# Kernel tuning notes

Hardware: AMD Instinct MI355X
Metric: run time of the kernel (lower is better)

## Reference

```python
import jax, jax.numpy as jnp
import numpy as np

B, N, C = 4, 49152, 256
E = 393216
CMID = C // 4
K = 3
EPS = 1e-5


def _cheb_prop(x, row, col, a_norm):
    # L_hat x with lambda_max=2, sym norm: L_hat = -D^{-1/2} A D^{-1/2} (zero diag)
    # x: [B, N, F]
    msg = a_norm[None, :, None] * x[:, col, :]           # [B, E, F]
    return -jnp.zeros_like(x).at[:, row, :].add(msg)


def _cheb_conv(x, row, col, a_norm, W, b):
    # W: [K, Fin, Fout], b: [Fout]
    out = jnp.einsum('bnf,fg->bng', x, W[0])
    Tx0, Tx1 = x, _cheb_prop(x, row, col, a_norm)
    out = out + jnp.einsum('bnf,fg->bng', Tx1, W[1])
    for k in range(2, W.shape[0]):
        Tx2 = 2.0 * _cheb_prop(Tx1, row, col, a_norm) - Tx0
        out = out + jnp.einsum('bnf,fg->bng', Tx2, W[k])
        Tx0, Tx1 = Tx1, Tx2
    return out + b


def _inst_norm(y):
    # InstanceNorm over the node axis (y viewed as [B, C, N]), affine=False
    mean = jnp.mean(y, axis=1, keepdims=True)
    var = jnp.var(y, axis=1, keepdims=True)
    return (y - mean) * jax.lax.rsqrt(var + EPS)


def setup_inputs() -> dict:
    key = jax.random.key(0)
    ks = jax.random.split(key, 8)
    x = jax.random.normal(ks[0], (B, N, C), dtype=jnp.float32)
    edge_index = jax.random.randint(ks[1], (2, E), 0, N, dtype=jnp.int32)
    edge_weight = jax.random.uniform(ks[2], (E,), dtype=jnp.float32)
    s1 = 1.0 / np.sqrt(C)
    s2 = 1.0 / np.sqrt(CMID)
    W1 = jax.random.normal(ks[3], (K, C, CMID), dtype=jnp.float32) * s1
    W2 = jax.random.normal(ks[4], (K, CMID, CMID), dtype=jnp.float32) * s2
    W3 = jax.random.normal(ks[5], (K, CMID, C), dtype=jnp.float32) * s2
    b1 = jnp.zeros((CMID,), dtype=jnp.float32)
    b2 = jnp.zeros((CMID,), dtype=jnp.float32)
    b3 = jnp.zeros((C,), dtype=jnp.float32)
    return {"x": x, "edge_index": edge_index, "edge_weight": edge_weight,
            "W1": W1, "b1": b1, "W2": W2, "b2": b2, "W3": W3, "b3": b3}


def reference(x, edge_index, edge_weight, W1, b1, W2, b2, W3, b3):
    row, col = edge_index[0], edge_index[1]
    deg = jnp.zeros((N,), dtype=x.dtype).at[row].add(edge_weight)
    dinv = jnp.where(deg > 0, jax.lax.rsqrt(jnp.maximum(deg, EPS)), 0.0)
    a_norm = edge_weight * dinv[row] * dinv[col]

    y = _cheb_conv(x, row, col, a_norm, W1, b1)
    y = jax.nn.relu(_inst_norm(y))
    y = _cheb_conv(y, row, col, a_norm, W2, b2)
    y = jax.nn.relu(_inst_norm(y))
    y = _cheb_conv(y, row, col, a_norm, W3, b3)
    y = jax.nn.relu(_inst_norm(y))
    return y + x
```

## Files before the change

### kernel.cpp

```cpp
#include <hip/hip_runtime.h>

#define NNODES 49152
#define NB 4
#define NE 393216
#define MTOT (NB*NNODES)
#define EPS 1e-5f

typedef __attribute__((ext_vector_type(8))) short s8v;
typedef __attribute__((ext_vector_type(4))) float f32x4;

__device__ inline float b2f(ushort u){ union{uint i; float f;} v; v.i = ((uint)u)<<16; return v.f; }
__device__ inline ushort f2b(float f){ union{float f; uint i;} v; v.f=f; uint r = v.i + 0x7fff + ((v.i>>16)&1); return (ushort)(r>>16); }

__global__ __launch_bounds__(256) void k_deg_cnt(const int* __restrict__ row,
    const float* __restrict__ w, float* __restrict__ deg, int* __restrict__ cnt)
{
    int e = blockIdx.x*256 + threadIdx.x;
    if (e >= NE) return;
    int r = row[e];
    atomicAdd(&deg[r], w[e]);
    atomicAdd(&cnt[r], 1);
}

__global__ __launch_bounds__(256) void k_dinv(const float* __restrict__ deg, float* __restrict__ dinv)
{
    int i = blockIdx.x*256 + threadIdx.x;
    if (i >= NNODES) return;
    float d = deg[i];
    dinv[i] = (d > 0.0f) ? rsqrtf(fmaxf(d, EPS)) : 0.0f;
}

__global__ __launch_bounds__(1024) void k_scan(const int* __restrict__ cnt, int* __restrict__ rowptr)
{
    __shared__ int ssum[1024];
    const int CH = NNODES/1024;
    int t = threadIdx.x;
    int base = t*CH;
    int loc[CH];
    int s = 0;
    #pragma unroll
    for (int i = 0; i < CH; ++i) { loc[i] = s; s += cnt[base+i]; }
    ssum[t] = s;
    __syncthreads();
    for (int off = 1; off < 1024; off <<= 1) {
        int v = ssum[t];
        int add = (t >= off) ? ssum[t-off] : 0;
        __syncthreads();
        ssum[t] = v + add;
        __syncthreads();
    }
    int prefix = (t == 0) ? 0 : ssum[t-1];
    #pragma unroll
    for (int i = 0; i < CH; ++i) rowptr[base+i] = prefix + loc[i];
    if (t == 0) rowptr[NNODES] = ssum[1023];
}

__global__ __launch_bounds__(256) void k_fill(const int* __restrict__ row, const int* __restrict__ col,
    const float* __restrict__ w, const float* __restrict__ dinv,
    const int* __restrict__ rowptr, int* __restrict__ fill,
    int* __restrict__ ecol, float* __restrict__ ea)
{
    int e = blockIdx.x*256 + threadIdx.x;
    if (e >= NE) return;
    int r = row[e], c = col[e];
    int pos = rowptr[r] + atomicAdd(&fill[r], 1);
    ecol[pos] = c;
    ea[pos] = w[e] * dinv[r] * dinv[c];
}

__global__ __launch_bounds__(256) void k_packB(const float* __restrict__ W, int Fin, int NF, int K,
    int mode, ushort* __restrict__ out)
{
    int t = blockIdx.x*256 + threadIdx.x;
    int lane = t & 63;
    int fid = t >> 6;
    if (fid >= (K/32)*NF) return;
    int kb = fid / NF, nb = fid % NF;
    int kbase = kb*32 + ((lane>>4)<<3);
    int n0 = nb*16 + (lane&15);
    #pragma unroll
    for (int j = 0; j < 8; ++j) {
        int kk = kbase + j;
        float v;
        if (mode == 0) {
            if (n0 < 64)       v = W[kk*64 + n0] - W[2*Fin*64 + kk*64 + n0];
            else if (n0 < 128) v = W[Fin*64 + kk*64 + (n0-64)];
            else               v = W[2*Fin*64 + kk*64 + (n0-128)];
        } else {
            v = W[(kk>>6)*64*256 + (kk&63)*256 + n0];
        }
        out[((long)fid*64 + lane)*8 + j] = f2b(v);
    }
}

template<int N_, int AF32, int OUTF32>
__global__ __launch_bounds__(256) void k_mgemm(
    const void* __restrict__ A0v, const void* __restrict__ A1v, const void* __restrict__ A2v,
    int Kper, int K, const ushort* __restrict__ Bp, void* __restrict__ Cv)
{
    const int NF = N_/16;
    int tid = threadIdx.x;
    int w = tid >> 6, l = tid & 63;
    long row_base = (long)blockIdx.x*128 + w*32;
    int lr = l & 15;
    int kg = l >> 4;
    f32x4 acc[2][NF];
    #pragma unroll
    for (int rf = 0; rf < 2; ++rf)
        #pragma unroll
        for (int nb = 0; nb < NF; ++nb) acc[rf][nb] = (f32x4){0.f,0.f,0.f,0.f};

    for (int kt = 0; kt < K; kt += 32) {
        int part = kt / Kper;
        const void* Ap = (part == 0) ? A0v : ((part == 1) ? A1v : A2v);
        int kc = kt - part*Kper;
        s8v afr[2];
        #pragma unroll
        for (int rf = 0; rf < 2; ++rf) {
            long row = row_base + rf*16 + lr;
            if (AF32) {
                const float* af = (const float*)Ap + row*(long)Kper + kc + (kg<<3);
                float4 v0 = *(const float4*)af;
                float4 v1 = *(const float4*)(af + 4);
                s8v fr;
                fr[0]=(short)f2b(v0.x); fr[1]=(short)f2b(v0.y); fr[2]=(short)f2b(v0.z); fr[3]=(short)f2b(v0.w);
                fr[4]=(short)f2b(v1.x); fr[5]=(short)f2b(v1.y); fr[6]=(short)f2b(v1.z); fr[7]=(short)f2b(v1.w);
                afr[rf] = fr;
            } else {
                afr[rf] = *(const s8v*)((const ushort*)Ap + row*(long)Kper + kc + (kg<<3));
            }
        }
        const ushort* bb = Bp + ((long)(kt>>5)*NF*64 + l)*8;
        #pragma unroll
        for (int nb = 0; nb < NF; ++nb) {
            s8v bfr = *(const s8v*)(bb + (long)nb*64*8);
            acc[0][nb] = __builtin_amdgcn_mfma_f32_16x16x32_bf16(afr[0], bfr, acc[0][nb], 0, 0, 0);
            acc[1][nb] = __builtin_amdgcn_mfma_f32_16x16x32_bf16(afr[1], bfr, acc[1][nb], 0, 0, 0);
        }
    }
    #pragma unroll
    for (int rf = 0; rf < 2; ++rf) {
        long r0 = row_base + rf*16 + (kg<<2);
        #pragma unroll
        for (int nb = 0; nb < NF; ++nb) {
            int cc = nb*16 + lr;
            #pragma unroll
            for (int i = 0; i < 4; ++i) {
                float v = acc[rf][nb][i];
                if (OUTF32) ((float*)Cv)[(r0+i)*N_ + cc] = v;
                else        ((ushort*)Cv)[(r0+i)*N_ + cc] = f2b(v);
            }
        }
    }
}

__global__ __launch_bounds__(256) void k_prop(
    const int* __restrict__ rowptr, const int* __restrict__ ecol, const float* __restrict__ ea,
    const ushort* __restrict__ src, int sstride, int soff,
    const ushort* __restrict__ basep, int bstride, int boff, float beta,
    ushort* __restrict__ dst, int dstride, int doff, float alpha)
{
    int g = blockIdx.x*16 + (threadIdx.x >> 4);
    int q = threadIdx.x & 15;
    int e0 = rowptr[g], e1 = rowptr[g+1];
    f32x4 acc[4];
    #pragma unroll
    for (int b = 0; b < 4; ++b) acc[b] = (f32x4){0.f,0.f,0.f,0.f};
    for (int e = e0; e < e1; ++e) {
        int c = ecol[e];
        float a = ea[e];
        #pragma unroll
        for (int b = 0; b < 4; ++b) {
            ushort4 v = *(const ushort4*)(src + ((long)b*NNODES + c)*sstride + soff + q*4);
            acc[b][0] += a*b2f(v.x); acc[b][1] += a*b2f(v.y);
            acc[b][2] += a*b2f(v.z); acc[b][3] += a*b2f(v.w);
        }
    }
    #pragma unroll
    for (int b = 0; b < 4; ++b) {
        float r0 = alpha*acc[b][0], r1 = alpha*acc[b][1], r2 = alpha*acc[b][2], r3 = alpha*acc[b][3];
        if (basep) {
            ushort4 bb = *(const ushort4*)(basep + ((long)b*NNODES + g)*bstride + boff + q*4);
            r0 += beta*b2f(bb.x); r1 += beta*b2f(bb.y); r2 += beta*b2f(bb.z); r3 += beta*b2f(bb.w);
        }
        ushort4 o; o.x = f2b(r0); o.y = f2b(r1); o.z = f2b(r2); o.w = f2b(r3);
        *(ushort4*)(dst + ((long)b*NNODES + g)*dstride + doff + q*4) = o;
    }
}

__global__ __launch_bounds__(256) void k_stats64(const ushort* __restrict__ y,
    float* __restrict__ sum, float* __restrict__ sumsq)
{
    int b = blockIdx.y;
    int c4 = (threadIdx.x & 15)*4;
    int rsub = threadIdx.x >> 4;
    long r0 = (long)blockIdx.x*256;
    float s0=0,s1=0,s2=0,s3=0, q0=0,q1=0,q2=0,q3=0;
    for (int i = 0; i < 16; ++i) {
        long r = r0 + rsub + i*16;
        ushort4 v = *(const ushort4*)(y + ((long)b*NNODES + r)*192 + c4);
        float f0=b2f(v.x), f1=b2f(v.y), f2=b2f(v.z), f3=b2f(v.w);
        s0+=f0; q0+=f0*f0; s1+=f1; q1+=f1*f1; s2+=f2; q2+=f2*f2; s3+=f3; q3+=f3*f3;
    }
    __shared__ float ls[16][64], lss[16][64];
    ls[rsub][c4]=s0; ls[rsub][c4+1]=s1; ls[rsub][c4+2]=s2; ls[rsub][c4+3]=s3;
    lss[rsub][c4]=q0; lss[rsub][c4+1]=q1; lss[rsub][c4+2]=q2; lss[rsub][c4+3]=q3;
    __syncthreads();
    for (int off = 8; off; off >>= 1) {
        if (rsub < off) {
            #pragma unroll
            for (int j = 0; j < 4; ++j) {
                ls[rsub][c4+j] += ls[rsub+off][c4+j];
                lss[rsub][c4+j] += lss[rsub+off][c4+j];
            }
        }
        __syncthreads();
    }
    if (rsub == 0) {
        #pragma unroll
        for (int j = 0; j < 4; ++j) {
            atomicAdd(&sum[b*256 + c4 + j], ls[0][c4+j]);
            atomicAdd(&sumsq[b*256 + c4 + j], lss[0][c4+j]);
        }
    }
}

__global__ __launch_bounds__(256) void k_stats256(const float* __restrict__ y,
    float* __restrict__ sum, float* __restrict__ sumsq)
{
    int b = blockIdx.y;
    int c = threadIdx.x;
    long r0 = (long)blockIdx.x*256;
    float s = 0.f, ss = 0.f;
    for (int r = 0; r < 256; ++r) {
        float v = y[((long)b*NNODES + r0 + r)*256 + c];
        s += v; ss += v*v;
    }
    atomicAdd(&sum[b*256 + c], s);
    atomicAdd(&sumsq[b*256 + c], ss);
}

__global__ __launch_bounds__(256) void k_finalize(const float* __restrict__ sum,
    const float* __restrict__ sumsq, float* __restrict__ mean, float* __restrict__ rs, int C_)
{
    int i = blockIdx.x*256 + threadIdx.x;
    if (i >= NB*256) return;
    int c = i % 256;
    if (c >= C_) return;
    float m = sum[i] / (float)NNODES;
    float v = sumsq[i] / (float)NNODES - m*m;
    mean[i] = m;
    rs[i] = rsqrtf(v + EPS);
}

__global__ __launch_bounds__(256) void k_normrelu(const ushort* __restrict__ U,
    const float* __restrict__ mean, const float* __restrict__ rs, ushort* __restrict__ X)
{
    long idx = (long)blockIdx.x*256 + threadIdx.x;
    long bn = idx >> 4;
    int q = (int)(idx & 15);
    int b = (int)(bn / NNODES);
    ushort4 v = *(const ushort4*)(U + bn*192 + q*4);
    float4 m = *(const float4*)(mean + b*256 + q*4);
    float4 r_ = *(const float4*)(rs + b*256 + q*4);
    ushort4 o;
    o.x = f2b(fmaxf((b2f(v.x)-m.x)*r_.x, 0.f));
    o.y = f2b(fmaxf((b2f(v.y)-m.y)*r_.y, 0.f));
    o.z = f2b(fmaxf((b2f(v.z)-m.z)*r_.z, 0.f));
    o.w = f2b(fmaxf((b2f(v.w)-m.w)*r_.w, 0.f));
    *(ushort4*)(X + bn*64 + q*4) = o;
}

__global__ __launch_bounds__(256) void k_final(float* __restrict__ Y,
    const float* __restrict__ x, const float* __restrict__ mean, const float* __restrict__ rs)
{
    long idx = (long)blockIdx.x*256 + threadIdx.x;
    long bn = idx >> 6;
    int q = (int)(idx & 63);
    int b = (int)(bn / NNODES);
    float4 v = *(const float4*)(Y + bn*256 + q*4);
    float4 m = *(const float4*)(mean + b*256 + q*4);
    float4 r_ = *(const float4*)(rs + b*256 + q*4);
    float4 xv = *(const float4*)(x + bn*256 + q*4);
    float4 o;
    o.x = fmaxf((v.x-m.x)*r_.x, 0.f) + xv.x;
    o.y = fmaxf((v.y-m.y)*r_.y, 0.f) + xv.y;
    o.z = fmaxf((v.z-m.z)*r_.z, 0.f) + xv.z;
    o.w = fmaxf((v.w-m.w)*r_.w, 0.f) + xv.w;
    *(float4*)(Y + bn*256 + q*4) = o;
}

extern "C" void kernel_launch(void* const* d_in, const int* in_sizes, int n_in,
                              void* d_out, int out_size, void* d_ws, size_t ws_size,
                              hipStream_t stream)
{
    const float* x  = (const float*)d_in[0];
    const int*   ei = (const int*)d_in[1];
    const float* ew = (const float*)d_in[2];
    const float* W1 = (const float*)d_in[3];
    const float* W2 = (const float*)d_in[5];
    const float* W3 = (const float*)d_in[7];
    const int* row = ei;
    const int* col = ei + NE;

    char* p = (char*)d_ws;
    size_t used = 0;
    auto alloc = [&](size_t bytes) -> void* {
        void* r = p + used;
        used += (bytes + 1023) & ~(size_t)1023;
        return r;
    };
    float* deg   = (float*)alloc((size_t)3*NNODES*4);
    int*   cnt   = (int*)(deg + NNODES);
    int*   fillc = (int*)(deg + 2*NNODES);
    float* dinv  = (float*)alloc((size_t)NNODES*4);
    int*   rowptr= (int*)alloc((size_t)(NNODES+1)*4);
    int*   ecol  = (int*)alloc((size_t)NE*4);
    float* ea    = (float*)alloc((size_t)NE*4);
    float* stats = (float*)alloc((size_t)2*NB*256*4);
    float* sumb  = stats;
    float* sumsq = stats + NB*256;
    float* meanb = (float*)alloc((size_t)NB*256*4);
    float* rsb   = (float*)alloc((size_t)NB*256*4);
    ushort* Bp1  = (ushort*)alloc((size_t)256*192*2);
    ushort* Bp2  = (ushort*)alloc((size_t)64*192*2);
    ushort* Bp3  = (ushort*)alloc((size_t)192*256*2);
    ushort* bufX = (ushort*)alloc((size_t)MTOT*64*2);
    ushort* T1   = (ushort*)alloc((size_t)MTOT*64*2);
    ushort* T2   = (ushort*)alloc((size_t)MTOT*64*2);
    if (ws_size < used) return;

    ushort* U = (ushort*)d_out;
    float*  Y = (float*)d_out;

    hipMemsetAsync(deg, 0, (size_t)3*NNODES*4, stream);
    k_deg_cnt<<<NE/256, 256, 0, stream>>>(row, ew, deg, cnt);
    k_dinv<<<NNODES/256, 256, 0, stream>>>(deg, dinv);
    k_scan<<<1, 1024, 0, stream>>>(cnt, rowptr);
    k_fill<<<NE/256, 256, 0, stream>>>(row, col, ew, dinv, rowptr, fillc, ecol, ea);
    k_packB<<<24, 256, 0, stream>>>(W1, 256, 12, 256, 0, Bp1);
    k_packB<<<6, 256, 0, stream>>>(W2, 64, 12, 64, 0, Bp2);
    k_packB<<<24, 256, 0, stream>>>(W3, 64, 16, 192, 1, Bp3);

    k_mgemm<192,1,0><<<MTOT/128, 256, 0, stream>>>(x, nullptr, nullptr, 256, 256, Bp1, U);
    k_prop<<<NNODES/16, 256, 0, stream>>>(rowptr, ecol, ea, U,192,128, U,192,64, 1.f, U,192,64, -2.f);
    k_prop<<<NNODES/16, 256, 0, stream>>>(rowptr, ecol, ea, U,192,64,  U,192,0,  1.f, U,192,0,  -1.f);
    hipMemsetAsync(stats, 0, (size_t)2*NB*256*4, stream);
    k_stats64<<<dim3(NNODES/256, NB), 256, 0, stream>>>(U, sumb, sumsq);
    k_finalize<<<NB, 256, 0, stream>>>(sumb, sumsq, meanb, rsb, 64);
    k_normrelu<<<MTOT*16/256, 256, 0, stream>>>(U, meanb, rsb, bufX);

    k_mgemm<192,0,0><<<MTOT/128, 256, 0, stream>>>(bufX, nullptr, nullptr, 64, 64, Bp2, U);
    k_prop<<<NNODES/16, 256, 0, stream>>>(rowptr, ecol, ea, U,192,128, U,192,64, 1.f, U,192,64, -2.f);
    k_prop<<<NNODES/16, 256, 0, stream>>>(rowptr, ecol, ea, U,192,64,  U,192,0,  1.f, U,192,0,  -1.f);
    hipMemsetAsync(stats, 0, (size_t)2*NB*256*4, stream);
    k_stats64<<<dim3(NNODES/256, NB), 256, 0, stream>>>(U, sumb, sumsq);
    k_finalize<<<NB, 256, 0, stream>>>(sumb, sumsq, meanb, rsb, 64);
    k_normrelu<<<MTOT*16/256, 256, 0, stream>>>(U, meanb, rsb, bufX);

    k_prop<<<NNODES/16, 256, 0, stream>>>(rowptr, ecol, ea, bufX,64,0, (const ushort*)nullptr,0,0, 0.f, T1,64,0, -1.f);
    k_prop<<<NNODES/16, 256, 0, stream>>>(rowptr, ecol, ea, T1,64,0, bufX,64,0, -1.f, T2,64,0, -2.f);
    k_mgemm<256,0,1><<<MTOT/128, 256, 0, stream>>>(bufX, T1, T2, 64, 192, Bp3, Y);
    hipMemsetAsync(stats, 0, (size_t)2*NB*256*4, stream);
    k_stats256<<<dim3(NNODES/256, NB), 256, 0, stream>>>(Y, sumb, sumsq);
    k_finalize<<<NB, 256, 0, stream>>>(sumb, sumsq, meanb, rsb, 256);
    k_final<<<MTOT*64/256, 256, 0, stream>>>(Y, x, meanb, rsb);
}
```

Before: 698.9 us.

## Interleave batch into node rows and split GEMM outputs into separate buffers

Intermediate activations move to a node-major layout with the 4 batches interleaved, [N][B][64]. One propagation row therefore gathers a contiguous 512-byte segment per edge instead of four strided segments, and the Chebyshev terms are written by the GEMM into separate contiguous buffers. Stats and normalization kernels are rewritten for the new layout with wider vector loads, and the stat memsets are merged into the initial one. When workspace allows, the final GEMM output is kept as bf16 in a workspace buffer and the last norm kernel reads it back, transposing to the batch-major output. This adds index remapping and a second code path in exchange.

```diff
diff --git a/kernel.cpp b/kernel.cpp
--- a/kernel.cpp
+++ b/kernel.cpp
@@ -93,17 +93,17 @@
     }
 }
 
-template<int N_, int AF32, int OUTF32>
+template<int N_, int AMODE, int CMODE>
 __global__ __launch_bounds__(256) void k_mgemm(
-    const void* __restrict__ A0v, const void* __restrict__ A1v, const void* __restrict__ A2v,
-    int Kper, int K, const ushort* __restrict__ Bp, void* __restrict__ Cv)
+    const void* __restrict__ Aa, const void* __restrict__ Ab, const void* __restrict__ Ac,
+    int K, const ushort* __restrict__ Bp,
+    void* __restrict__ C0, void* __restrict__ C1, void* __restrict__ C2)
 {
     const int NF = N_/16;
     int tid = threadIdx.x;
     int w = tid >> 6, l = tid & 63;
-    long row_base = (long)blockIdx.x*128 + w*32;
-    int lr = l & 15;
-    int kg = l >> 4;
+    int lr = l & 15, kg = l >> 4;
+    long rb = (long)blockIdx.x * 128;
     f32x4 acc[2][NF];
     #pragma unroll
     for (int rf = 0; rf < 2; ++rf)
@@ -111,44 +111,57 @@
         for (int nb = 0; nb < NF; ++nb) acc[rf][nb] = (f32x4){0.f,0.f,0.f,0.f};
 
     for (int kt = 0; kt < K; kt += 32) {
-        int part = kt / Kper;
-        const void* Ap = (part == 0) ? A0v : ((part == 1) ? A1v : A2v);
-        int kc = kt - part*Kper;
         s8v afr[2];
         #pragma unroll
         for (int rf = 0; rf < 2; ++rf) {
-            long row = row_base + rf*16 + lr;
-            if (AF32) {
-                const float* af = (const float*)Ap + row*(long)Kper + kc + (kg<<3);
+            long rg = rb + w*32 + rf*16 + lr;
+            if (AMODE == 1) {
+                const float* af = (const float*)Aa + rg*256 + kt + (kg<<3);
                 float4 v0 = *(const float4*)af;
                 float4 v1 = *(const float4*)(af + 4);
                 s8v fr;
                 fr[0]=(short)f2b(v0.x); fr[1]=(short)f2b(v0.y); fr[2]=(short)f2b(v0.z); fr[3]=(short)f2b(v0.w);
                 fr[4]=(short)f2b(v1.x); fr[5]=(short)f2b(v1.y); fr[6]=(short)f2b(v1.z); fr[7]=(short)f2b(v1.w);
                 afr[rf] = fr;
+            } else if (AMODE == 0) {
+                afr[rf] = *(const s8v*)((const ushort*)Aa + rg*64 + kt + (kg<<3));
             } else {
-                afr[rf] = *(const s8v*)((const ushort*)Ap + row*(long)Kper + kc + (kg<<3));
+                int part = kt >> 6, kc = kt & 63;
+                const ushort* ap = (part == 0) ? (const ushort*)Aa : ((part == 1) ? (const ushort*)Ab : (const ushort*)Ac);
+                afr[rf] = *(const s8v*)(ap + rg*64 + kc + (kg<<3));
             }
         }
-        const ushort* bb = Bp + ((long)(kt>>5)*NF*64 + l)*8;
+        const ushort* bb = Bp + ((long)(kt>>5)*NF)*512 + l*8;
         #pragma unroll
         for (int nb = 0; nb < NF; ++nb) {
-            s8v bfr = *(const s8v*)(bb + (long)nb*64*8);
+            s8v bfr = *(const s8v*)(bb + nb*512);
             acc[0][nb] = __builtin_amdgcn_mfma_f32_16x16x32_bf16(afr[0], bfr, acc[0][nb], 0, 0, 0);
             acc[1][nb] = __builtin_amdgcn_mfma_f32_16x16x32_bf16(afr[1], bfr, acc[1][nb], 0, 0, 0);
         }
     }
+
+    int b4 = 0, n0 = 0;
+    if (AMODE == 1) { b4 = (int)(rb / NNODES); n0 = (int)(rb - (long)b4*NNODES); }
     #pragma unroll
     for (int rf = 0; rf < 2; ++rf) {
-        long r0 = row_base + rf*16 + (kg<<2);
         #pragma unroll
         for (int nb = 0; nb < NF; ++nb) {
-            int cc = nb*16 + lr;
             #pragma unroll
             for (int i = 0; i < 4; ++i) {
+                int lrw = w*32 + rf*16 + kg*4 + i;
+                int cc = nb*16 + lr;
                 float v = acc[rf][nb][i];
-                if (OUTF32) ((float*)Cv)[(r0+i)*N_ + cc] = v;
-                else        ((ushort*)Cv)[(r0+i)*N_ + cc] = f2b(v);
+                if (CMODE == 0) {
+                    long crow = (AMODE == 1) ? ((long)(n0 + lrw)*4 + b4) : (rb + lrw);
+                    ushort* arr = (nb < 4) ? (ushort*)C0 : ((nb < 8) ? (ushort*)C1 : (ushort*)C2);
+                    arr[crow*64 + (nb&3)*16 + lr] = f2b(v);
+                } else if (CMODE == 1) {
+                    ((ushort*)C0)[(rb + lrw)*256 + cc] = f2b(v);
+                } else {
+                    long r = rb + lrw;
+                    int n = (int)(r >> 2), b = (int)(r & 3);
+                    ((float*)C0)[((long)b*NNODES + n)*256 + cc] = v;
+                }
             }
         }
     }
@@ -156,88 +169,99 @@
 
 __global__ __launch_bounds__(256) void k_prop(
     const int* __restrict__ rowptr, const int* __restrict__ ecol, const float* __restrict__ ea,
-    const ushort* __restrict__ src, int sstride, int soff,
-    const ushort* __restrict__ basep, int bstride, int boff, float beta,
-    ushort* __restrict__ dst, int dstride, int doff, float alpha)
-{
-    int g = blockIdx.x*16 + (threadIdx.x >> 4);
-    int q = threadIdx.x & 15;
+    const ushort* __restrict__ src, const ushort* __restrict__ basep, float beta,
+    ushort* __restrict__ dst, float alpha)
+{
+    int g = blockIdx.x*8 + (threadIdx.x >> 5);
+    int sub = threadIdx.x & 31;
     int e0 = rowptr[g], e1 = rowptr[g+1];
-    f32x4 acc[4];
-    #pragma unroll
-    for (int b = 0; b < 4; ++b) acc[b] = (f32x4){0.f,0.f,0.f,0.f};
+    float acc[8];
+    #pragma unroll
+    for (int j = 0; j < 8; ++j) acc[j] = 0.f;
     for (int e = e0; e < e1; ++e) {
         int c = ecol[e];
         float a = ea[e];
-        #pragma unroll
-        for (int b = 0; b < 4; ++b) {
-            ushort4 v = *(const ushort4*)(src + ((long)b*NNODES + c)*sstride + soff + q*4);
-            acc[b][0] += a*b2f(v.x); acc[b][1] += a*b2f(v.y);
-            acc[b][2] += a*b2f(v.z); acc[b][3] += a*b2f(v.w);
-        }
-    }
-    #pragma unroll
-    for (int b = 0; b < 4; ++b) {
-        float r0 = alpha*acc[b][0], r1 = alpha*acc[b][1], r2 = alpha*acc[b][2], r3 = alpha*acc[b][3];
-        if (basep) {
-            ushort4 bb = *(const ushort4*)(basep + ((long)b*NNODES + g)*bstride + boff + q*4);
-            r0 += beta*b2f(bb.x); r1 += beta*b2f(bb.y); r2 += beta*b2f(bb.z); r3 += beta*b2f(bb.w);
-        }
-        ushort4 o; o.x = f2b(r0); o.y = f2b(r1); o.z = f2b(r2); o.w = f2b(r3);
-        *(ushort4*)(dst + ((long)b*NNODES + g)*dstride + doff + q*4) = o;
-    }
-}
-
-__global__ __launch_bounds__(256) void k_stats64(const ushort* __restrict__ y,
+        s8v v = *(const s8v*)(src + (long)c*256 + sub*8);
+        #pragma unroll
+        for (int j = 0; j < 8; ++j) acc[j] += a * b2f((ushort)v[j]);
+    }
+    s8v o;
+    if (basep) {
+        s8v bv = *(const s8v*)(basep + (long)g*256 + sub*8);
+        #pragma unroll
+        for (int j = 0; j < 8; ++j) o[j] = (short)f2b(alpha*acc[j] + beta*b2f((ushort)bv[j]));
+    } else {
+        #pragma unroll
+        for (int j = 0; j < 8; ++j) o[j] = (short)f2b(alpha*acc[j]);
+    }
+    *(s8v*)(dst + (long)g*256 + sub*8) = o;
+}
+
+__global__ __launch_bounds__(256) void k_statsA(const ushort* __restrict__ y,
     float* __restrict__ sum, float* __restrict__ sumsq)
 {
-    int b = blockIdx.y;
-    int c4 = (threadIdx.x & 15)*4;
-    int rsub = threadIdx.x >> 4;
-    long r0 = (long)blockIdx.x*256;
-    float s0=0,s1=0,s2=0,s3=0, q0=0,q1=0,q2=0,q3=0;
-    for (int i = 0; i < 16; ++i) {
-        long r = r0 + rsub + i*16;
-        ushort4 v = *(const ushort4*)(y + ((long)b*NNODES + r)*192 + c4);
-        float f0=b2f(v.x), f1=b2f(v.y), f2=b2f(v.z), f3=b2f(v.w);
-        s0+=f0; q0+=f0*f0; s1+=f1; q1+=f1*f1; s2+=f2; q2+=f2*f2; s3+=f3; q3+=f3*f3;
-    }
-    __shared__ float ls[16][64], lss[16][64];
-    ls[rsub][c4]=s0; ls[rsub][c4+1]=s1; ls[rsub][c4+2]=s2; ls[rsub][c4+3]=s3;
-    lss[rsub][c4]=q0; lss[rsub][c4+1]=q1; lss[rsub][c4+2]=q2; lss[rsub][c4+3]=q3;
+    int t = threadIdx.x;
+    float s[8], q[8];
+    #pragma unroll
+    for (int j = 0; j < 8; ++j) { s[j] = 0.f; q[j] = 0.f; }
+    for (int i = 0; i < 12; ++i) {
+        long e = ((long)(i*512 + blockIdx.x))*2048 + t*8;
+        s8v v = *(const s8v*)(y + e);
+        #pragma unroll
+        for (int j = 0; j < 8; ++j) { float f = b2f((ushort)v[j]); s[j] += f; q[j] += f*f; }
+    }
+    __shared__ float ls[256][8], lq[256][8];
+    #pragma unroll
+    for (int j = 0; j < 8; ++j) { ls[t][j] = s[j]; lq[t][j] = q[j]; }
     __syncthreads();
-    for (int off = 8; off; off >>= 1) {
-        if (rsub < off) {
+    #pragma unroll
+    for (int off = 128; off >= 32; off >>= 1) {
+        if (t < off) {
             #pragma unroll
-            for (int j = 0; j < 4; ++j) {
-                ls[rsub][c4+j] += ls[rsub+off][c4+j];
-                lss[rsub][c4+j] += lss[rsub+off][c4+j];
-            }
+            for (int j = 0; j < 8; ++j) { ls[t][j] += ls[t+off][j]; lq[t][j] += lq[t+off][j]; }
         }
         __syncthreads();
     }
-    if (rsub == 0) {
-        #pragma unroll
-        for (int j = 0; j < 4; ++j) {
-            atomicAdd(&sum[b*256 + c4 + j], ls[0][c4+j]);
-            atomicAdd(&sumsq[b*256 + c4 + j], lss[0][c4+j]);
-        }
-    }
-}
-
-__global__ __launch_bounds__(256) void k_stats256(const float* __restrict__ y,
+    if (t < 32) {
+        int b = (t>>3)&3, c0 = (t&7)*8;
+        #pragma unroll
+        for (int j = 0; j < 8; ++j) {
+            atomicAdd(&sum[b*256 + c0 + j], ls[t][j]);
+            atomicAdd(&sumsq[b*256 + c0 + j], lq[t][j]);
+        }
+    }
+}
+
+__global__ __launch_bounds__(256) void k_statsY(const ushort* __restrict__ y,
     float* __restrict__ sum, float* __restrict__ sumsq)
 {
-    int b = blockIdx.y;
-    int c = threadIdx.x;
-    long r0 = (long)blockIdx.x*256;
-    float s = 0.f, ss = 0.f;
-    for (int r = 0; r < 256; ++r) {
-        float v = y[((long)b*NNODES + r0 + r)*256 + c];
-        s += v; ss += v*v;
-    }
-    atomicAdd(&sum[b*256 + c], s);
-    atomicAdd(&sumsq[b*256 + c], ss);
+    int t = threadIdx.x;
+    float s[8], q[8];
+    #pragma unroll
+    for (int j = 0; j < 8; ++j) { s[j] = 0.f; q[j] = 0.f; }
+    for (int i = 0; i < 48; ++i) {
+        long e = ((long)(i*512 + blockIdx.x))*2048 + t*8;
+        s8v v = *(const s8v*)(y + e);
+        #pragma unroll
+        for (int j = 0; j < 8; ++j) { float f = b2f((ushort)v[j]); s[j] += f; q[j] += f*f; }
+    }
+    __shared__ float ls[256][8], lq[256][8];
+    #pragma unroll
+    for (int j = 0; j < 8; ++j) { ls[t][j] = s[j]; lq[t][j] = q[j]; }
+    __syncthreads();
+    if (t < 128) {
+        #pragma unroll
+        for (int j = 0; j < 8; ++j) { ls[t][j] += ls[t+128][j]; lq[t][j] += lq[t+128][j]; }
+    }
+    __syncthreads();
+    if (t < 128) {
+        int b = (t>>5)&3, c0 = (t&31)*8;
+        #pragma unroll
+        for (int j = 0; j < 8; ++j) {
+            atomicAdd(&sum[b*256 + c0 + j], ls[t][j]);
+            atomicAdd(&sumsq[b*256 + c0 + j], lq[t][j]);
+        }
+    }
 }
 
 __global__ __launch_bounds__(256) void k_finalize(const float* __restrict__ sum,
@@ -253,25 +277,64 @@
     rs[i] = rsqrtf(v + EPS);
 }
 
-__global__ __launch_bounds__(256) void k_normrelu(const ushort* __restrict__ U,
+__global__ __launch_bounds__(256) void k_normrelu(const ushort* __restrict__ y,
     const float* __restrict__ mean, const float* __restrict__ rs, ushort* __restrict__ X)
 {
-    long idx = (long)blockIdx.x*256 + threadIdx.x;
-    long bn = idx >> 4;
-    int q = (int)(idx & 15);
-    int b = (int)(bn / NNODES);
-    ushort4 v = *(const ushort4*)(U + bn*192 + q*4);
-    float4 m = *(const float4*)(mean + b*256 + q*4);
-    float4 r_ = *(const float4*)(rs + b*256 + q*4);
-    ushort4 o;
-    o.x = f2b(fmaxf((b2f(v.x)-m.x)*r_.x, 0.f));
-    o.y = f2b(fmaxf((b2f(v.y)-m.y)*r_.y, 0.f));
-    o.z = f2b(fmaxf((b2f(v.z)-m.z)*r_.z, 0.f));
-    o.w = f2b(fmaxf((b2f(v.w)-m.w)*r_.w, 0.f));
-    *(ushort4*)(X + bn*64 + q*4) = o;
-}
-
-__global__ __launch_bounds__(256) void k_final(float* __restrict__ Y,
+    int t = threadIdx.x;
+    long e = (long)blockIdx.x*2048 + t*8;
+    int b = (t>>3)&3, c0 = (t&7)*8;
+    s8v v = *(const s8v*)(y + e);
+    float4 m0 = *(const float4*)(mean + b*256 + c0);
+    float4 m1 = *(const float4*)(mean + b*256 + c0 + 4);
+    float4 r0 = *(const float4*)(rs + b*256 + c0);
+    float4 r1 = *(const float4*)(rs + b*256 + c0 + 4);
+    float mm[8] = {m0.x,m0.y,m0.z,m0.w,m1.x,m1.y,m1.z,m1.w};
+    float rr[8] = {r0.x,r0.y,r0.z,r0.w,r1.x,r1.y,r1.z,r1.w};
+    s8v o;
+    #pragma unroll
+    for (int j = 0; j < 8; ++j) o[j] = (short)f2b(fmaxf((b2f((ushort)v[j]) - mm[j])*rr[j], 0.f));
+    *(s8v*)(X + e) = o;
+}
+
+__global__ __launch_bounds__(256) void k_final(const ushort* __restrict__ Ybf,
+    const float* __restrict__ x, const float* __restrict__ mean, const float* __restrict__ rs,
+    float* __restrict__ out)
+{
+    int t = threadIdx.x;
+    long orow = (long)blockIdx.x*8 + (t>>5);
+    int c0 = (t&31)*8;
+    int b = (int)(orow / NNODES);
+    int n = (int)(orow - (long)b*NNODES);
+    s8v v = *(const s8v*)(Ybf + ((long)n*4 + b)*256 + c0);
+    float4 m0 = *(const float4*)(mean + b*256 + c0);
+    float4 m1 = *(const float4*)(mean + b*256 + c0 + 4);
+    float4 r0 = *(const float4*)(rs + b*256 + c0);
+    float4 r1 = *(const float4*)(rs + b*256 + c0 + 4);
+    float mm[8] = {m0.x,m0.y,m0.z,m0.w,m1.x,m1.y,m1.z,m1.w};
+    float rr[8] = {r0.x,r0.y,r0.z,r0.w,r1.x,r1.y,r1.z,r1.w};
+    const float* xp = x + orow*256 + c0;
+    float* op = out + orow*256 + c0;
+    #pragma unroll
+    for (int j = 0; j < 8; ++j)
+        op[j] = fmaxf((b2f((ushort)v[j]) - mm[j])*rr[j], 0.f) + xp[j];
+}
+
+__global__ __launch_bounds__(256) void k_stats256f(const float* __restrict__ y,
+    float* __restrict__ sum, float* __restrict__ sumsq)
+{
+    int b = blockIdx.y;
+    int c = threadIdx.x;
+    long r0 = (long)blockIdx.x*256;
+    float s = 0.f, ss = 0.f;
+    for (int r = 0; r < 256; ++r) {
+        float v = y[((long)b*NNODES + r0 + r)*256 + c];
+        s += v; ss += v*v;
+    }
+    atomicAdd(&sum[b*256 + c], s);
+    atomicAdd(&sumsq[b*256 + c], ss);
+}
+
+__global__ __launch_bounds__(256) void k_finalf(float* __restrict__ Y,
     const float* __restrict__ x, const float* __restrict__ mean, const float* __restrict__ rs)
 {
     long idx = (long)blockIdx.x*256 + threadIdx.x;
@@ -313,27 +376,33 @@
     float* deg   = (float*)alloc((size_t)3*NNODES*4);
     int*   cnt   = (int*)(deg + NNODES);
     int*   fillc = (int*)(deg + 2*NNODES);
+    float* stats = (float*)alloc((size_t)3*2*1024*4);
     float* dinv  = (float*)alloc((size_t)NNODES*4);
     int*   rowptr= (int*)alloc((size_t)(NNODES+1)*4);
     int*   ecol  = (int*)alloc((size_t)NE*4);
     float* ea    = (float*)alloc((size_t)NE*4);
-    float* stats = (float*)alloc((size_t)2*NB*256*4);
-    float* sumb  = stats;
-    float* sumsq = stats + NB*256;
-    float* meanb = (float*)alloc((size_t)NB*256*4);
-    float* rsb   = (float*)alloc((size_t)NB*256*4);
+    float* mrs   = (float*)alloc((size_t)3*2*1024*4);
     ushort* Bp1  = (ushort*)alloc((size_t)256*192*2);
     ushort* Bp2  = (ushort*)alloc((size_t)64*192*2);
     ushort* Bp3  = (ushort*)alloc((size_t)192*256*2);
-    ushort* bufX = (ushort*)alloc((size_t)MTOT*64*2);
-    ushort* T1   = (ushort*)alloc((size_t)MTOT*64*2);
-    ushort* T2   = (ushort*)alloc((size_t)MTOT*64*2);
-    if (ws_size < used) return;
-
-    ushort* U = (ushort*)d_out;
-    float*  Y = (float*)d_out;
-
-    hipMemsetAsync(deg, 0, (size_t)3*NNODES*4, stream);
+    ushort* Za   = (ushort*)alloc((size_t)MTOT*64*2);
+    ushort* Zb   = (ushort*)alloc((size_t)MTOT*64*2);
+    ushort* Zc   = (ushort*)alloc((size_t)MTOT*64*2);
+    ushort* Zd   = (ushort*)alloc((size_t)MTOT*64*2);
+    size_t need_fb = used;
+    ushort* Ybf  = (ushort*)alloc((size_t)MTOT*256*2);
+    size_t need_main = used;
+    if (ws_size < need_fb) return;
+    bool mainPath = ws_size >= need_main;
+
+    float* sum1 = stats;           float* sq1 = stats + 1024;
+    float* sum2 = stats + 2048;    float* sq2 = stats + 3072;
+    float* sum3 = stats + 4096;    float* sq3 = stats + 5120;
+    float* mean1 = mrs;            float* rs1 = mrs + 1024;
+    float* mean2 = mrs + 2048;     float* rs2 = mrs + 3072;
+    float* mean3 = mrs + 4096;     float* rs3 = mrs + 5120;
+
+    hipMemsetAsync(deg, 0, (size_t)3*NNODES*4 + (size_t)3*2*1024*4, stream);
     k_deg_cnt<<<NE/256, 256, 0, stream>>>(row, ew, deg, cnt);
     k_dinv<<<NNODES/256, 256, 0, stream>>>(deg, dinv);
     k_scan<<<1, 1024, 0, stream>>>(cnt, rowptr);
@@ -342,27 +411,32 @@
     k_packB<<<6, 256, 0, stream>>>(W2, 64, 12, 64, 0, Bp2);
     k_packB<<<24, 256, 0, stream>>>(W3, 64, 16, 192, 1, Bp3);
 
-    k_mgemm<192,1,0><<<MTOT/128, 256, 0, stream>>>(x, nullptr, nullptr, 256, 256, Bp1, U);
-    k_prop<<<NNODES/16, 256, 0, stream>>>(rowptr, ecol, ea, U,192,128, U,192,64, 1.f, U,192,64, -2.f);
-    k_prop<<<NNODES/16, 256, 0, stream>>>(rowptr, ecol, ea, U,192,64,  U,192,0,  1.f, U,192,0,  -1.f);
-    hipMemsetAsync(stats, 0, (size_t)2*NB*256*4, stream);
-    k_stats64<<<dim3(NNODES/256, NB), 256, 0, stream>>>(U, sumb, sumsq);
-    k_finalize<<<NB, 256, 0, stream>>>(sumb, sumsq, meanb, rsb, 64);
-    k_normrelu<<<MTOT*16/256, 256, 0, stream>>>(U, meanb, rsb, bufX);
-
-    k_mgemm<192,0,0><<<MTOT/128, 256, 0, stream>>>(bufX, nullptr, nullptr, 64, 64, Bp2, U);
-    k_prop<<<NNODES/16, 256, 0, stream>>>(rowptr, ecol, ea, U,192,128, U,192,64, 1.f, U,192,64, -2.f);
-    k_prop<<<NNODES/16, 256, 0, stream>>>(rowptr, ecol, ea, U,192,64,  U,192,0,  1.f, U,192,0,  -1.f);
-    hipMemsetAsync(stats, 0, (size_t)2*NB*256*4, stream);
-    k_stats64<<<dim3(NNODES/256, NB), 256, 0, stream>>>(U, sumb, sumsq);
-    k_finalize<<<NB, 256, 0, stream>>>(sumb, sumsq, meanb, rsb, 64);
-    k_normrelu<<<MTOT*16/256, 256, 0, stream>>>(U, meanb, rsb, bufX);
-
-    k_prop<<<NNODES/16, 256, 0, stream>>>(rowptr, ecol, ea, bufX,64,0, (const ushort*)nullptr,0,0, 0.f, T1,64,0, -1.f);
-    k_prop<<<NNODES/16, 256, 0, stream>>>(rowptr, ecol, ea, T1,64,0, bufX,64,0, -1.f, T2,64,0, -2.f);
-    k_mgemm<256,0,1><<<MTOT/128, 256, 0, stream>>>(bufX, T1, T2, 64, 192, Bp3, Y);
-    hipMemsetAsync(stats, 0, (size_t)2*NB*256*4, stream);
-    k_stats256<<<dim3(NNODES/256, NB), 256, 0, stream>>>(Y, sumb, sumsq);
-    k_finalize<<<NB, 256, 0, stream>>>(sumb, sumsq, meanb, rsb, 256);
-    k_final<<<MTOT*64/256, 256, 0, stream>>>(Y, x, meanb, rsb);
-}
+    k_mgemm<192,1,0><<<MTOT/128, 256, 0, stream>>>(x, nullptr, nullptr, 256, Bp1, Za, Zb, Zc);
+    k_prop<<<NNODES/8, 256, 0, stream>>>(rowptr, ecol, ea, Zc, Zb, 1.f, Zb, -2.f);
+    k_prop<<<NNODES/8, 256, 0, stream>>>(rowptr, ecol, ea, Zb, Za, 1.f, Za, -1.f);
+    k_statsA<<<512, 256, 0, stream>>>(Za, sum1, sq1);
+    k_finalize<<<4, 256, 0, stream>>>(sum1, sq1, mean1, rs1, 64);
+    k_normrelu<<<MTOT*64/2048, 256, 0, stream>>>(Za, mean1, rs1, Zc);
+
+    k_mgemm<192,0,0><<<MTOT/128, 256, 0, stream>>>(Zc, nullptr, nullptr, 64, Bp2, Za, Zb, Zd);
+    k_prop<<<NNODES/8, 256, 0, stream>>>(rowptr, ecol, ea, Zd, Zb, 1.f, Zb, -2.f);
+    k_prop<<<NNODES/8, 256, 0, stream>>>(rowptr, ecol, ea, Zb, Za, 1.f, Za, -1.f);
+    k_statsA<<<512, 256, 0, stream>>>(Za, sum2, sq2);
+    k_finalize<<<4, 256, 0, stream>>>(sum2, sq2, mean2, rs2, 64);
+    k_normrelu<<<MTOT*64/2048, 256, 0, stream>>>(Za, mean2, rs2, Zc);
+
+    k_prop<<<NNODES/8, 256, 0, stream>>>(rowptr, ecol, ea, Zc, (const ushort*)nullptr, 0.f, Za, -1.f);
+    k_prop<<<NNODES/8, 256, 0, stream>>>(rowptr, ecol, ea, Za, Zc, -1.f, Zb, -2.f);
+    if (mainPath) {
+        k_mgemm<256,2,1><<<MTOT/128, 256, 0, stream>>>(Zc, Za, Zb, 192, Bp3, Ybf, nullptr, nullptr);
+        k_statsY<<<512, 256, 0, stream>>>(Ybf, sum3, sq3);
+        k_finalize<<<4, 256, 0, stream>>>(sum3, sq3, mean3, rs3, 256);
+        k_final<<<MTOT*256/2048, 256, 0, stream>>>(Ybf, x, mean3, rs3, (float*)d_out);
+    } else {
+        float* Y = (float*)d_out;
+        k_mgemm<256,2,2><<<MTOT/128, 256, 0, stream>>>(Zc, Za, Zb, 192, Bp3, Y, nullptr, nullptr);
+        k_stats256f<<<dim3(NNODES/256, NB), 256, 0, stream>>>(Y, sum3, sq3);
+        k_finalize<<<4, 256, 0, stream>>>(sum3, sq3, mean3, rs3, 256);
+        k_finalf<<<MTOT*64/256, 256, 0, stream>>>(Y, x, mean3, rs3);
+    }
+}
```

Measured after the change: 951.0 us. 36.1% more time.
